# Kernel tuning notes

Hardware: AMD Instinct MI355X
Metric: run time of the kernel (lower is better)

Reference implementation:

```python
import jax, jax.numpy as jnp
import numpy as np

D, B, L, E, H, F = 6, 4, 2048, 1024, 16, 4096
DH = E // H
DECAY = 16.0
CSCALE = 1.0
EPS = 1e-5


def _ln(x, w, b):
    m = jnp.mean(x, axis=-1, keepdims=True)
    v = jnp.mean(jnp.square(x - m), axis=-1, keepdims=True)
    return (x - m) * jax.lax.rsqrt(v + EPS) * w + b


def setup_inputs() -> dict:
    key = jax.random.key(0)
    ks = jax.random.split(key, 10)
    s = 0.02
    f32 = jnp.float32
    return {
        "x": jax.random.normal(ks[0], (B, L, E), f32),
        "Wq": jax.random.normal(ks[1], (D, E, E), f32) * s,
        "Wk": jax.random.normal(ks[2], (D, E, E), f32) * s,
        "bq": jnp.zeros((D, E), f32),
        "bk": jnp.zeros((D, E), f32),
        "ln1_w": jnp.ones((D, E), f32), "ln1_b": jnp.zeros((D, E), f32),
        "ln2_w": jnp.ones((D, E), f32), "ln2_b": jnp.zeros((D, E), f32),
        "ln3_w": jnp.ones((D, E), f32), "ln3_b": jnp.zeros((D, E), f32),
        "W1": jax.random.normal(ks[3], (D, F, E), f32) * s,
        "b1": jnp.zeros((D, F), f32),
        "W2": jax.random.normal(ks[4], (D, E, F), f32) * s,
        "b2": jnp.zeros((D, E), f32),
    }


def reference(x, Wq, Wk, bq, bk, ln1_w, ln1_b, ln2_w, ln2_b, ln3_w, ln3_b, W1, b1, W2, b2):
    seq = x.shape[1]
    pos = jnp.arange(seq)
    # exponential relative-position bias exp(-|i-j|/decay), shared by all layers
    rel = jnp.exp(-jnp.abs(pos[:, None] - pos[None, :]).astype(x.dtype) / DECAY)
    inv_sqrt_d = 1.0 / np.sqrt(DH)

    def layer(h, p):
        (wq, wk, bq_, bk_, l1w, l1b, l2w, l2b, l3w, l3b, w1, b1_, w2, b2_) = p
        bh, sl, _ = h.shape
        q = (h @ wq.T + bq_).reshape(bh, sl, H, DH)
        k = (h @ wk.T + bk_).reshape(bh, sl, H, DH)
        scores = jnp.einsum('blhd,bmhd->bhlm', q, k) * inv_sqrt_d
        # torch MHA need_weights=True averages softmax weights over heads
        w_avg = jax.nn.softmax(scores, axis=-1).mean(axis=1)  # [B,L,L]
        new_w = jax.nn.softmax(CSCALE * w_avg + rel[None], axis=-1)
        sa = jnp.einsum('blm,bme->ble', new_w, h)  # value = raw residual stream
        h1 = _ln(h + sa, l1w, l1b)
        h2 = _ln(h1, l2w, l2b)  # Noop cross-attn block (LayerNorm scale-invariant)
        ff = jax.nn.relu(h2 @ w1.T + b1_) @ w2.T + b2_
        return _ln(h2 + ff, l3w, l3b), None

    out, _ = jax.lax.scan(layer, x, (Wq, Wk, bq, bk, ln1_w, ln1_b, ln2_w, ln2_b,
                                     ln3_w, ln3_b, W1, b1, W2, b2))
    return out
```

## Files before the change

### kernel.cpp

```cpp
#include <hip/hip_runtime.h>

#define D_ 6
#define B_ 4
#define L_ 2048
#define E_ 1024
#define H_ 16
#define F_ 4096
#define BL_ (B_ * L_)
#define QKS 2048
#define EPS_ 1e-5f
#define EXPSC 0.18033688011112042f
#define LOG2E 1.4426950408889634f
#define LOG2E_H (LOG2E / 16.0f)

typedef __bf16 bf16x8 __attribute__((ext_vector_type(8)));
typedef __bf16 bf16x4 __attribute__((ext_vector_type(4)));
typedef float f32x4 __attribute__((ext_vector_type(4)));

__device__ __forceinline__ float fexp2(float x) {
  return __builtin_amdgcn_exp2f(x);
}

__device__ __forceinline__ void gload_lds16(const void* g, void* l) {
  __builtin_amdgcn_global_load_lds(
      (const __attribute__((address_space(1))) void*)g,
      (__attribute__((address_space(3))) void*)l, 16, 0, 0);
}

__device__ __forceinline__ void stage_tile64_512(__bf16* ldsb,
                                                 const __bf16* gbase, long ldg,
                                                 int tid) {
  int row = tid >> 3, cu = tid & 7;
  const __bf16* src = gbase + (long)row * ldg + ((cu ^ (row & 7)) << 3);
  gload_lds16(src, ldsb + (long)((tid & ~63) << 3));
}

__device__ __forceinline__ void stage_tile128_512(__bf16* ldsb,
                                                  const __bf16* gbase,
                                                  long ldg, int tid) {
#pragma unroll
  for (int j = 0; j < 2; ++j) {
    int unit = j * 512 + tid;
    int row = unit >> 3, cu = unit & 7;
    const __bf16* src = gbase + (long)row * ldg + ((cu ^ (row & 7)) << 3);
    gload_lds16(src, ldsb + (long)((j * 512 + (tid & ~63)) << 3));
  }
}

#define RD_FRAG(ldsb, r_, kk) \
  (*(const bf16x8*)&(ldsb)[((r_) * 8 + (((kk) * 4 + l4) ^ ((r_) & 7))) * 8])

#define LDA_SUB(P, MH)                                                        \
  _Pragma("unroll") for (int mi = 0; mi < 4; ++mi)                            \
  _Pragma("unroll") for (int kk = 0; kk < 2; ++kk) {                          \
    int r_ = wr + (MH) * 64 + mi * 16 + l15;                                  \
    int cu_ = kk * 4 + l4;                                                    \
    aF[mi][kk] = *(const bf16x8*)&lds[P][0][(r_ * 8 + (cu_ ^ (r_ & 7))) * 8]; \
  }

#define LDB_SUB(P, BF, NH)                                                    \
  _Pragma("unroll") for (int ni = 0; ni < 2; ++ni)                            \
  _Pragma("unroll") for (int kk = 0; kk < 2; ++kk) {                          \
    int r_ = wc + (NH) * 32 + ni * 16 + l15;                                  \
    int cu_ = kk * 4 + l4;                                                    \
    BF[ni][kk] = *(const bf16x8*)&lds[P][1][(r_ * 8 + (cu_ ^ (r_ & 7))) * 8]; \
  }

#define MFMA_Q(AF, BF, MH, NH)                                                \
  _Pragma("unroll") for (int mi = 0; mi < 4; ++mi)                            \
  _Pragma("unroll") for (int ni = 0; ni < 2; ++ni)                            \
  _Pragma("unroll") for (int kk = 0; kk < 2; ++kk)                            \
    acc[(MH) * 4 + mi][(NH) * 2 + ni] =                                       \
        __builtin_amdgcn_mfma_f32_16x16x32_bf16(                              \
            AF[mi][kk], BF[ni][kk], acc[(MH) * 4 + mi][(NH) * 2 + ni], 0, 0, 0);

#define PHASE_PRE()                                                           \
  __builtin_amdgcn_s_barrier();                                               \
  asm volatile("s_waitcnt lgkmcnt(0)" ::: "memory");                          \
  __builtin_amdgcn_sched_barrier(0);                                          \
  __builtin_amdgcn_s_setprio(1)

#define PHASE_POST()                                                          \
  __builtin_amdgcn_s_setprio(0);                                              \
  __builtin_amdgcn_sched_barrier(0);                                          \
  __builtin_amdgcn_s_barrier()

#define STAGE_A(BUFI, HF, K0)                                                 \
  do {                                                                        \
    gload_lds16(sA[HF][0] + (K0),                                             \
                &lds[BUFI][0][((HF) * 1024 + wave * 64) * 8]);                \
    gload_lds16(sA[HF][1] + (K0),                                             \
                &lds[BUFI][0][((HF) * 1024 + 512 + wave * 64) * 8]);          \
  } while (0)

#define STAGE_B(BUFI, HF, K0)                                                 \
  do {                                                                        \
    gload_lds16(sB[HF][0] + (K0),                                             \
                &lds[BUFI][1][((HF) * 1024 + wave * 64) * 8]);                \
    gload_lds16(sB[HF][1] + (K0),                                             \
                &lds[BUFI][1][((HF) * 1024 + 512 + wave * 64) * 8]);          \
  } while (0)

template <int EPI>
__global__ __launch_bounds__(512, 2) void gemm8p(
    const __bf16* __restrict__ A, const __bf16* __restrict__ Bm,
    __bf16* __restrict__ Cb, const float* __restrict__ bias, int M, int N,
    int K, int lda, int ldb, int zk, long strA, long strB, long strC,
    long strCk) {
  __shared__ __bf16 lds[2][2][256 * 64];
  const int tid = threadIdx.x;
  const int wave = tid >> 6, lane = tid & 63;
  const int l15 = lane & 15, l4 = lane >> 4;
  const int z = blockIdx.y;
  const int kc = (zk == 2) ? (z & 1) : 0;
  const int bat = (zk == 2) ? (z >> 1) : z;
  const __bf16* Ab = A + (long)bat * strA + (long)kc * K;
  const __bf16* Bb = Bm + (long)bat * strB + (long)kc * K;
  const long coff = (long)bat * strC + (long)kc * strCk;

  const int nbx = N >> 8;
  const int nwg = (M >> 8) * nbx;
  const int orig = blockIdx.x;
  const int qq = nwg >> 3, rr = nwg & 7;
  const int xcd = orig & 7, lid = orig >> 3;
  const int wg = (xcd < rr ? xcd * (qq + 1) : rr * (qq + 1) + (xcd - rr) * qq) + lid;
  const int row0 = (wg / nbx) * 256, col0 = (wg % nbx) * 256;
  const int wr = (wave >> 2) * 128;
  const int wc = (wave & 3) * 64;

  const int rsel = tid >> 3;
  const int swz = ((lane & 7) ^ (rsel & 7)) << 3;
  const __bf16* sA[2][2];
  const __bf16* sB[2][2];
#pragma unroll
  for (int hf = 0; hf < 2; ++hf)
#pragma unroll
    for (int j = 0; j < 2; ++j) {
      sA[hf][j] = Ab + (long)(row0 + hf * 128 + j * 64 + rsel) * lda + swz;
      sB[hf][j] = Bb + (long)(col0 + hf * 128 + j * 64 + rsel) * ldb + swz;
    }

  const int NT = K >> 6;
  STAGE_A(0, 0, 0);
  STAGE_A(0, 1, 0);
  STAGE_B(0, 0, 0);
  STAGE_B(0, 1, 0);
  STAGE_A(1, 0, 64);
  STAGE_B(1, 0, 64);
  STAGE_A(1, 1, 64);
  asm volatile("s_waitcnt vmcnt(6)" ::: "memory");
  __builtin_amdgcn_s_barrier();

  f32x4 acc[8][4];
#pragma unroll
  for (int i = 0; i < 8; ++i)
#pragma unroll
    for (int j = 0; j < 4; ++j) acc[i][j] = (f32x4){0.f, 0.f, 0.f, 0.f};
  bf16x8 aF[4][2], b0F[2][2], b1F[2][2];

  for (int t = 0; t < NT; ++t) {
    const int p = t & 1;
    const int kA = (t + 1 < NT ? t + 1 : NT - 1) << 6;
    const int kB = (t + 2 < NT ? t + 2 : NT - 1) << 6;
    LDA_SUB(p, 0);
    LDB_SUB(p, b0F, 0);
    STAGE_B(p ^ 1, 1, kA);
    PHASE_PRE();
    MFMA_Q(aF, b0F, 0, 0);
    PHASE_POST();
    LDB_SUB(p, b1F, 1);
    PHASE_PRE();
    MFMA_Q(aF, b1F, 0, 1);
    PHASE_POST();
    LDA_SUB(p, 1);
    STAGE_B(p, 0, kB);
    PHASE_PRE();
    MFMA_Q(aF, b0F, 1, 0);
    PHASE_POST();
    STAGE_A(p, 0, kB);
    STAGE_A(p, 1, kB);
    __builtin_amdgcn_s_barrier();
    __builtin_amdgcn_sched_barrier(0);
    __builtin_amdgcn_s_setprio(1);
    MFMA_Q(aF, b1F, 1, 1);
    __builtin_amdgcn_s_setprio(0);
    __builtin_amdgcn_sched_barrier(0);
    asm volatile("s_waitcnt vmcnt(6)" ::: "memory");
    __builtin_amdgcn_s_barrier();
  }
  asm volatile("s_waitcnt vmcnt(0)" ::: "memory");

#pragma unroll
  for (int i = 0; i < 8; ++i) {
    int row = row0 + wr + (i >> 2) * 64 + (i & 3) * 16 + l4 * 4;
#pragma unroll
    for (int j = 0; j < 4; ++j) {
      int col = col0 + wc + (j >> 1) * 32 + (j & 1) * 16 + l15;
      float bval = 0.f;
      if constexpr (EPI == 1 || EPI == 2) bval = bias[col];
#pragma unroll
      for (int r = 0; r < 4; ++r) {
        long crow = row + r;
        float v = acc[i][j][r];
        if constexpr (EPI == 1 || EPI == 2) v += bval;
        if constexpr (EPI == 2) v = fmaxf(v, 0.f);
        Cb[coff + crow * N + col] = (__bf16)v;
      }
    }
  }
}

__global__ __launch_bounds__(512, 4) void attn_stats_kernel(
    const __bf16* __restrict__ qk, float* __restrict__ sinv) {
  __shared__ __bf16 sK[2][64 * 64];
  const int tid = threadIdx.x, wave = tid >> 6, lane = tid & 63;
  const int l15 = lane & 15, l4 = lane >> 4;
  const int l0 = blockIdx.x * 128, h = blockIdx.y, b = blockIdx.z;
  const __bf16* Kb = qk + ((long)b * L_) * QKS + 1024 + h * 64;

  const __bf16* qp =
      qk + ((long)(b * L_ + l0 + wave * 16 + l15)) * QKS + h * 64 + l4 * 8;
  const bf16x8 aF0 = *(const bf16x8*)qp;
  const bf16x8 aF1 = *(const bf16x8*)(qp + 32);

  stage_tile64_512(sK[0], Kb, QKS, tid);
  asm volatile("s_waitcnt vmcnt(0)" ::: "memory");
  __builtin_amdgcn_s_barrier();

  float msum[4] = {0.f, 0.f, 0.f, 0.f};
  int p = 0;
  for (int m0 = 0; m0 < 32; ++m0) {
    const int mn = (m0 + 1 < 32) ? m0 + 1 : 31;
    stage_tile64_512(sK[p ^ 1], Kb + (long)mn * 64 * QKS, QKS, tid);
    asm volatile("s_waitcnt vmcnt(1)" ::: "memory");
    __builtin_amdgcn_s_barrier();
#pragma unroll
    for (int ni = 0; ni < 4; ++ni) {
      const int rB = ni * 16 + l15;
      bf16x8 b0 = RD_FRAG(sK[p], rB, 0);
      bf16x8 b1 = RD_FRAG(sK[p], rB, 1);
      f32x4 s = (f32x4){0.f, 0.f, 0.f, 0.f};
      s = __builtin_amdgcn_mfma_f32_16x16x32_bf16(aF0, b0, s, 0, 0, 0);
      s = __builtin_amdgcn_mfma_f32_16x16x32_bf16(aF1, b1, s, 0, 0, 0);
#pragma unroll
      for (int r = 0; r < 4; ++r) msum[r] += fexp2(s[r]);
    }
    asm volatile("" ::: "memory");
    __builtin_amdgcn_s_barrier();
    p ^= 1;
  }
#pragma unroll
  for (int r = 0; r < 4; ++r) {
    float s = msum[r];
    for (int d = 1; d < 16; d <<= 1) s += __shfl_xor(s, d, 64);
    msum[r] = s;
  }
  if (l15 == 0) {
    long idx = ((long)(b * H_ + h)) * L_ + l0 + wave * 16 + l4 * 4;
    f32x4 o = {1.0f / msum[0], 1.0f / msum[1], 1.0f / msum[2], 1.0f / msum[3]};
    *(f32x4*)&sinv[idx] = o;
  }
}

__global__ __launch_bounds__(512, 2) void attn_probs_kernel(
    const __bf16* __restrict__ qk, const float* __restrict__ sinv,
    const float* __restrict__ relTab, __bf16* __restrict__ P,
    float* __restrict__ rowsumT) {
  __shared__ __bf16 sKl[2][128 * 64];
  const int tid = threadIdx.x, wave = tid >> 6, lane = tid & 63;
  const int l15 = lane & 15, l4 = lane >> 4;
  const int m0 = blockIdx.x * 128, l0 = blockIdx.y * 128, b = blockIdx.z;
  const int wr2 = wave & 3, wc2 = wave >> 2;
  const __bf16* Kb = qk + ((long)(b * L_ + m0)) * QKS + 1024;

  const int rowbase = l0 + wr2 * 32 + l4 * 4;
  const __bf16* qp0 =
      qk + ((long)(b * L_ + l0 + wr2 * 32 + l15)) * QKS + l4 * 8;
  const __bf16* qp1 = qp0 + 16 * QKS;

  stage_tile128_512(sKl[0], Kb, QKS, tid);

  float wacc[4][8];
#pragma unroll
  for (int i = 0; i < 4; ++i)
#pragma unroll
    for (int j = 0; j < 8; ++j) wacc[i][j] = 0.f;

  int p = 0;
  for (int h = 0; h < H_; ++h) {
    bf16x8 aF[2][2];
    aF[0][0] = *(const bf16x8*)(qp0 + h * 64);
    aF[0][1] = *(const bf16x8*)(qp0 + h * 64 + 32);
    aF[1][0] = *(const bf16x8*)(qp1 + h * 64);
    aF[1][1] = *(const bf16x8*)(qp1 + h * 64 + 32);
    const float* svh = &sinv[((long)(b * H_ + h)) * L_];
    f32x4 iv0 = *(const f32x4*)&svh[rowbase];
    f32x4 iv1 = *(const f32x4*)&svh[rowbase + 16];
    const int hn = (h + 1 < H_) ? h + 1 : H_ - 1;
    stage_tile128_512(sKl[p ^ 1], Kb + hn * 64, QKS, tid);
    asm volatile("s_waitcnt vmcnt(2)" ::: "memory");
    __builtin_amdgcn_s_barrier();
#pragma unroll
    for (int ni = 0; ni < 4; ++ni) {
      const int rB = wc2 * 64 + ni * 16 + l15;
      bf16x8 b0 = RD_FRAG(sKl[p], rB, 0);
      bf16x8 b1 = RD_FRAG(sKl[p], rB, 1);
#pragma unroll
      for (int fi = 0; fi < 2; ++fi) {
        f32x4 s = (f32x4){0.f, 0.f, 0.f, 0.f};
        s = __builtin_amdgcn_mfma_f32_16x16x32_bf16(aF[fi][0], b0, s, 0, 0, 0);
        s = __builtin_amdgcn_mfma_f32_16x16x32_bf16(aF[fi][1], b1, s, 0, 0, 0);
#pragma unroll
        for (int r = 0; r < 4; ++r)
          wacc[ni][fi * 4 + r] += fexp2(s[r]) * (fi ? iv1[r] : iv0[r]);
      }
    }
    asm volatile("" ::: "memory");
    __builtin_amdgcn_s_barrier();
    p ^= 1;
  }
  float rowpart[2][4] = {{0.f, 0.f, 0.f, 0.f}, {0.f, 0.f, 0.f, 0.f}};
#pragma unroll
  for (int ni = 0; ni < 4; ++ni) {
#pragma unroll
    for (int fi = 0; fi < 2; ++fi) {
#pragma unroll
      for (int r = 0; r < 4; ++r) {
        int row = rowbase + fi * 16 + r;
        int col = m0 + wc2 * 64 + ni * 16 + l15;
        float relL = relTab[row - col + 2048];
        float pv = fexp2(fmaf(wacc[ni][fi * 4 + r], LOG2E_H, relL));
        P[((long)b * L_ + row) * L_ + col] = (__bf16)pv;
        rowpart[fi][r] += pv;
      }
    }
  }
#pragma unroll
  for (int fi = 0; fi < 2; ++fi) {
#pragma unroll
    for (int r = 0; r < 4; ++r) {
      float s = rowpart[fi][r];
      s += __shfl_xor(s, 1, 16);
      s += __shfl_xor(s, 2, 16);
      s += __shfl_xor(s, 4, 16);
      s += __shfl_xor(s, 8, 16);
      if (l15 == 0) {
        int row = rowbase + fi * 16 + r;
        rowsumT[((long)b * L_ + row) * 32 + (m0 >> 6) + wc2] = s;
      }
    }
  }
}

__device__ __forceinline__ void wave_reduce2(float& a, float& b) {
#pragma unroll
  for (int d = 1; d < 64; d <<= 1) {
    a += __shfl_xor(a, d, 64);
    b += __shfl_xor(b, d, 64);
  }
}

__global__ __launch_bounds__(256, 4) void ln12_kernel(
    const float* __restrict__ hin, const __bf16* __restrict__ p0,
    const __bf16* __restrict__ p1, const float* __restrict__ rowsumT,
    const float* __restrict__ w1, const float* __restrict__ b1,
    const float* __restrict__ w2, const float* __restrict__ b2,
    float* __restrict__ h2f, __bf16* __restrict__ h2b) {
  __shared__ float sh[9];
  const int tid = threadIdx.x;
  const long row = blockIdx.x;
  const long base = row * E_ + tid * 4;
  if (tid < 32) {
    float s = rowsumT[row * 32 + tid];
#pragma unroll
    for (int d = 1; d < 32; d <<= 1) s += __shfl_xor(s, d, 32);
    if (tid == 0) sh[8] = s;
  }
  f32x4 hv = *(const f32x4*)&hin[base];
  bf16x4 p0v = *(const bf16x4*)&p0[base];
  bf16x4 p1v = *(const bf16x4*)&p1[base];
  __syncthreads();
  const float rinv = 1.0f / sh[8];
  float y[4];
  float s1 = 0.f, s2 = 0.f;
#pragma unroll
  for (int j = 0; j < 4; ++j) {
    y[j] = hv[j] + rinv * ((float)p0v[j] + (float)p1v[j]);
    s1 += y[j];
    s2 += y[j] * y[j];
  }
  wave_reduce2(s1, s2);
  if ((tid & 63) == 0) { sh[(tid >> 6) * 2] = s1; sh[(tid >> 6) * 2 + 1] = s2; }
  __syncthreads();
  s1 = sh[0] + sh[2] + sh[4] + sh[6];
  s2 = sh[1] + sh[3] + sh[5] + sh[7];
  float mean = s1 * (1.f / E_);
  float var = s2 * (1.f / E_) - mean * mean;
  float rs = rsqrtf(var + EPS_);
  f32x4 wv = *(const f32x4*)&w1[tid * 4];
  f32x4 bv = *(const f32x4*)&b1[tid * 4];
  float h1[4];
  s1 = 0.f; s2 = 0.f;
#pragma unroll
  for (int j = 0; j < 4; ++j) {
    h1[j] = (y[j] - mean) * rs * wv[j] + bv[j];
    s1 += h1[j];
    s2 += h1[j] * h1[j];
  }
  __syncthreads();
  wave_reduce2(s1, s2);
  if ((tid & 63) == 0) { sh[(tid >> 6) * 2] = s1; sh[(tid >> 6) * 2 + 1] = s2; }
  __syncthreads();
  s1 = sh[0] + sh[2] + sh[4] + sh[6];
  s2 = sh[1] + sh[3] + sh[5] + sh[7];
  mean = s1 * (1.f / E_);
  var = s2 * (1.f / E_) - mean * mean;
  rs = rsqrtf(var + EPS_);
  wv = *(const f32x4*)&w2[tid * 4];
  bv = *(const f32x4*)&b2[tid * 4];
  f32x4 o;
  bf16x4 ob;
#pragma unroll
  for (int j = 0; j < 4; ++j) {
    float v = (h1[j] - mean) * rs * wv[j] + bv[j];
    o[j] = v;
    ob[j] = (__bf16)v;
  }
  *(f32x4*)&h2f[base] = o;
  *(bf16x4*)&h2b[base] = ob;
}

__global__ __launch_bounds__(256, 4) void ln3_kernel(
    const float* __restrict__ h2f, const __bf16* __restrict__ p0,
    const __bf16* __restrict__ p1, const float* __restrict__ bias2,
    const float* __restrict__ w3, const float* __restrict__ b3,
    float* __restrict__ outf, __bf16* __restrict__ outb) {
  __shared__ float sh[8];
  const int tid = threadIdx.x;
  const long row = blockIdx.x;
  const long base = row * E_ + tid * 4;
  f32x4 hv = *(const f32x4*)&h2f[base];
  bf16x4 p0v = *(const bf16x4*)&p0[base];
  bf16x4 p1v = *(const bf16x4*)&p1[base];
  f32x4 b2v = *(const f32x4*)&bias2[tid * 4];
  float y[4];
  float s1 = 0.f, s2 = 0.f;
#pragma unroll
  for (int j = 0; j < 4; ++j) {
    y[j] = hv[j] + (float)p0v[j] + (float)p1v[j] + b2v[j];
    s1 += y[j];
    s2 += y[j] * y[j];
  }
  wave_reduce2(s1, s2);
  if ((tid & 63) == 0) { sh[(tid >> 6) * 2] = s1; sh[(tid >> 6) * 2 + 1] = s2; }
  __syncthreads();
  s1 = sh[0] + sh[2] + sh[4] + sh[6];
  s2 = sh[1] + sh[3] + sh[5] + sh[7];
  float mean = s1 * (1.f / E_);
  float var = s2 * (1.f / E_) - mean * mean;
  float rs = rsqrtf(var + EPS_);
  f32x4 wv = *(const f32x4*)&w3[tid * 4];
  f32x4 bv = *(const f32x4*)&b3[tid * 4];
  f32x4 o;
  bf16x4 ob;
#pragma unroll
  for (int j = 0; j < 4; ++j) {
    float v = (y[j] - mean) * rs * wv[j] + bv[j];
    o[j] = v;
    ob[j] = (__bf16)v;
  }
  *(f32x4*)&outf[base] = o;
  *(bf16x4*)&outb[base] = ob;
}

__global__ __launch_bounds__(256, 4) void transpose_kernel(
    const __bf16* __restrict__ X, __bf16* __restrict__ XT) {
  __shared__ __bf16 t[64 * 66];
  const int l0 = blockIdx.x * 64, e0 = blockIdx.y * 64, b = blockIdx.z;
  const int tid = threadIdx.x;
#pragma unroll
  for (int r = 0; r < 2; ++r) {
    int c = tid + 256 * r;
    int rw = c >> 3, c8 = (c & 7) * 8;
    *(bf16x8*)&t[rw * 66 + c8] =
        *(const bf16x8*)&X[((long)(b * L_) + l0 + rw) * E_ + e0 + c8];
  }
  __syncthreads();
#pragma unroll
  for (int r = 0; r < 2; ++r) {
    int c = tid + 256 * r;
    int er = c >> 3, l8 = (c & 7) * 8;
    bf16x8 v;
#pragma unroll
    for (int j = 0; j < 8; ++j) v[j] = t[(l8 + j) * 66 + er];
    *(bf16x8*)&XT[((long)(b * E_) + e0 + er) * L_ + l0 + l8] = v;
  }
}

__global__ __launch_bounds__(256, 4) void f32_to_bf16_kernel(
    const float* __restrict__ x, __bf16* __restrict__ y) {
  long i = ((long)blockIdx.x * 256 + threadIdx.x) * 4;
  f32x4 v = *(const f32x4*)&x[i];
  bf16x4 o;
#pragma unroll
  for (int j = 0; j < 4; ++j) o[j] = (__bf16)v[j];
  *(bf16x4*)&y[i] = o;
}

__global__ __launch_bounds__(256, 4) void build_wqk_kernel(
    const float* __restrict__ Wq, const float* __restrict__ Wk,
    __bf16* __restrict__ out) {
  long i = ((long)blockIdx.x * 256 + threadIdx.x) * 4;
  long d = i >> 21;
  long rem = i & ((1L << 21) - 1);
  long row = rem >> 10, col = rem & 1023;
  const bool isQ = (row < 1024);
  const float* src = isQ ? &Wq[(d << 20) + (row << 10) + col]
                         : &Wk[(d << 20) + ((row - 1024) << 10) + col];
  const float sc = isQ ? EXPSC : 1.0f;
  f32x4 v = *(const f32x4*)src;
  bf16x4 o;
#pragma unroll
  for (int j = 0; j < 4; ++j) o[j] = (__bf16)(v[j] * sc);
  *(bf16x4*)&out[i] = o;
}

__global__ __launch_bounds__(256, 4) void build_bqk_kernel(
    const float* __restrict__ bq, const float* __restrict__ bk,
    float* __restrict__ out) {
  int i = blockIdx.x * 256 + threadIdx.x;
  int d = i >> 11, c = i & 2047;
  out[i] = (c < 1024) ? bq[d * 1024 + c] * EXPSC : bk[d * 1024 + c - 1024];
}

__global__ __launch_bounds__(256, 4) void build_rel_kernel(
    float* __restrict__ relTab) {
  int i = blockIdx.x * 256 + threadIdx.x;
  relTab[i] = __expf(-fabsf((float)(i - 2048)) * (1.0f / 16.0f)) * LOG2E;
}

extern "C" void kernel_launch(void* const* d_in, const int* in_sizes, int n_in,
                              void* d_out, int out_size, void* d_ws,
                              size_t ws_size, hipStream_t stream) {
  const float* x = (const float*)d_in[0];
  const float* Wq = (const float*)d_in[1];
  const float* Wk = (const float*)d_in[2];
  const float* bq = (const float*)d_in[3];
  const float* bk = (const float*)d_in[4];
  const float* l1w = (const float*)d_in[5];
  const float* l1b = (const float*)d_in[6];
  const float* l2w = (const float*)d_in[7];
  const float* l2b = (const float*)d_in[8];
  const float* l3w = (const float*)d_in[9];
  const float* l3b = (const float*)d_in[10];
  const float* W1 = (const float*)d_in[11];
  const float* b1 = (const float*)d_in[12];
  const float* W2 = (const float*)d_in[13];
  const float* b2 = (const float*)d_in[14];

  char* p = (char*)d_ws;
  auto take = [&](size_t bytes) -> char* {
    char* r = p;
    p += (bytes + 255) & ~(size_t)255;
    return r;
  };
  __bf16* wqk_bf = (__bf16*)take((size_t)D_ * 2048 * 1024 * 2);
  __bf16* w1_bf = (__bf16*)take((size_t)D_ * F_ * E_ * 2);
  __bf16* w2_bf = (__bf16*)take((size_t)D_ * E_ * F_ * 2);
  __bf16* h_bf = (__bf16*)take((size_t)BL_ * E_ * 2);
  __bf16* hT = (__bf16*)take((size_t)BL_ * E_ * 2);
  __bf16* qk_bf = (__bf16*)take((size_t)BL_ * QKS * 2);
  __bf16* Pbuf = (__bf16*)take((size_t)B_ * L_ * L_ * 2);
  __bf16* ffmid = qk_bf;
  float* bqk = (float*)take((size_t)D_ * 2048 * 4);
  float* relTab = (float*)take((size_t)4096 * 4);
  float* sinv = (float*)take((size_t)B_ * H_ * L_ * 4);
  float* rowsumT = (float*)take((size_t)BL_ * 32 * 4);
  __bf16* partB = (__bf16*)take((size_t)2 * BL_ * E_ * 2);
  __bf16* part0 = partB;
  __bf16* part1 = partB + (size_t)BL_ * E_;
  float* hbuf = (float*)take((size_t)BL_ * E_ * 4);

  build_wqk_kernel<<<D_ * 2048 * 1024 / 1024, 256, 0, stream>>>(Wq, Wk, wqk_bf);
  build_bqk_kernel<<<D_ * 2048 / 256, 256, 0, stream>>>(bq, bk, bqk);
  build_rel_kernel<<<16, 256, 0, stream>>>(relTab);
  f32_to_bf16_kernel<<<D_ * F_ * E_ / 1024, 256, 0, stream>>>(W1, w1_bf);
  f32_to_bf16_kernel<<<D_ * E_ * F_ / 1024, 256, 0, stream>>>(W2, w2_bf);
  f32_to_bf16_kernel<<<BL_ * E_ / 1024, 256, 0, stream>>>(x, h_bf);
  transpose_kernel<<<dim3(L_ / 64, E_ / 64, B_), 256, 0, stream>>>(h_bf, hT);

  const float* h_in = x;
  for (int d = 0; d < D_; ++d) {
    gemm8p<1><<<dim3(256, 1), 512, 0, stream>>>(
        h_bf, wqk_bf + (size_t)d * 2048 * 1024, qk_bf, bqk + d * 2048, BL_,
        2048, E_, E_, E_, 1, 0, 0, 0, 0);
    attn_stats_kernel<<<dim3(L_ / 128, H_, B_), 512, 0, stream>>>(qk_bf, sinv);
    attn_probs_kernel<<<dim3(L_ / 128, L_ / 128, B_), 512, 0, stream>>>(
        qk_bf, sinv, relTab, Pbuf, rowsumT);
    gemm8p<0><<<dim3(32, 8), 512, 0, stream>>>(
        Pbuf, hT, partB, nullptr, L_, E_, L_ / 2, L_, L_, 2, (long)L_ * L_,
        (long)E_ * L_, (long)L_ * E_, (long)BL_ * E_);
    ln12_kernel<<<BL_, 256, 0, stream>>>(h_in, part0, part1, rowsumT,
                                         l1w + d * E_, l1b + d * E_,
                                         l2w + d * E_, l2b + d * E_, hbuf,
                                         h_bf);
    gemm8p<2><<<dim3(512, 1), 512, 0, stream>>>(
        h_bf, w1_bf + (size_t)d * F_ * E_, ffmid, b1 + d * F_, BL_, F_, E_,
        E_, E_, 1, 0, 0, 0, 0);
    gemm8p<0><<<dim3(128, 2), 512, 0, stream>>>(
        ffmid, w2_bf + (size_t)d * E_ * F_, partB, nullptr, BL_, E_, F_ / 2,
        F_, F_, 2, 0, 0, 0, (long)BL_ * E_);
    float* outp = (d == D_ - 1) ? (float*)d_out : hbuf;
    ln3_kernel<<<BL_, 256, 0, stream>>>(hbuf, part0, part1, b2 + d * E_,
                                        l3w + d * E_, l3b + d * E_, outp,
                                        h_bf);
    if (d < D_ - 1) {
      transpose_kernel<<<dim3(L_ / 64, E_ / 64, B_), 256, 0, stream>>>(h_bf, hT);
      h_in = hbuf;
    }
  }
}
```

Baseline: 2.379 ms.

## Stage Q tiles through LDS in attn_probs and drop fp32 h2 residual buffer

The attention-probability kernel now double-buffers Q head slices into shared memory alongside K, replacing strided per-lane global loads of Q fragments with async LDS staging. Separately, ln12 no longer writes an fp32 copy of h2, and ln3 reads the bf16 h2 for the residual instead. This cuts global traffic in both places. The cost is doubled LDS use in attn_probs, which may reduce occupancy, and lower precision of the residual in the final layer norm.

```diff
diff --git a/kernel.cpp b/kernel.cpp
--- a/kernel.cpp
+++ b/kernel.cpp
@@ -266,40 +266,41 @@
     const __bf16* __restrict__ qk, const float* __restrict__ sinv,
     const float* __restrict__ relTab, __bf16* __restrict__ P,
     float* __restrict__ rowsumT) {
+  __shared__ __bf16 sQ[2][128 * 64];
   __shared__ __bf16 sKl[2][128 * 64];
   const int tid = threadIdx.x, wave = tid >> 6, lane = tid & 63;
   const int l15 = lane & 15, l4 = lane >> 4;
   const int m0 = blockIdx.x * 128, l0 = blockIdx.y * 128, b = blockIdx.z;
   const int wr2 = wave & 3, wc2 = wave >> 2;
+  const __bf16* Qb = qk + ((long)(b * L_ + l0)) * QKS;
   const __bf16* Kb = qk + ((long)(b * L_ + m0)) * QKS + 1024;
 
+  stage_tile128_512(sQ[0], Qb, QKS, tid);
+  stage_tile128_512(sKl[0], Kb, QKS, tid);
+
+  float wacc[4][8];
+#pragma unroll
+  for (int i = 0; i < 4; ++i)
+#pragma unroll
+    for (int j = 0; j < 8; ++j) wacc[i][j] = 0.f;
+
+  const int rA0 = wr2 * 32 + l15;
   const int rowbase = l0 + wr2 * 32 + l4 * 4;
-  const __bf16* qp0 =
-      qk + ((long)(b * L_ + l0 + wr2 * 32 + l15)) * QKS + l4 * 8;
-  const __bf16* qp1 = qp0 + 16 * QKS;
-
-  stage_tile128_512(sKl[0], Kb, QKS, tid);
-
-  float wacc[4][8];
-#pragma unroll
-  for (int i = 0; i < 4; ++i)
-#pragma unroll
-    for (int j = 0; j < 8; ++j) wacc[i][j] = 0.f;
-
   int p = 0;
   for (int h = 0; h < H_; ++h) {
-    bf16x8 aF[2][2];
-    aF[0][0] = *(const bf16x8*)(qp0 + h * 64);
-    aF[0][1] = *(const bf16x8*)(qp0 + h * 64 + 32);
-    aF[1][0] = *(const bf16x8*)(qp1 + h * 64);
-    aF[1][1] = *(const bf16x8*)(qp1 + h * 64 + 32);
+    const int hn = (h + 1 < H_) ? h + 1 : H_ - 1;
+    stage_tile128_512(sQ[p ^ 1], Qb + hn * 64, QKS, tid);
+    stage_tile128_512(sKl[p ^ 1], Kb + hn * 64, QKS, tid);
     const float* svh = &sinv[((long)(b * H_ + h)) * L_];
     f32x4 iv0 = *(const f32x4*)&svh[rowbase];
     f32x4 iv1 = *(const f32x4*)&svh[rowbase + 16];
-    const int hn = (h + 1 < H_) ? h + 1 : H_ - 1;
-    stage_tile128_512(sKl[p ^ 1], Kb + hn * 64, QKS, tid);
-    asm volatile("s_waitcnt vmcnt(2)" ::: "memory");
+    asm volatile("s_waitcnt vmcnt(4)" ::: "memory");
     __builtin_amdgcn_s_barrier();
+    bf16x8 aF[2][2];
+    aF[0][0] = RD_FRAG(sQ[p], rA0, 0);
+    aF[0][1] = RD_FRAG(sQ[p], rA0, 1);
+    aF[1][0] = RD_FRAG(sQ[p], rA0 + 16, 0);
+    aF[1][1] = RD_FRAG(sQ[p], rA0 + 16, 1);
 #pragma unroll
     for (int ni = 0; ni < 4; ++ni) {
       const int rB = wc2 * 64 + ni * 16 + l15;
@@ -365,7 +366,7 @@
     const __bf16* __restrict__ p1, const float* __restrict__ rowsumT,
     const float* __restrict__ w1, const float* __restrict__ b1,
     const float* __restrict__ w2, const float* __restrict__ b2,
-    float* __restrict__ h2f, __bf16* __restrict__ h2b) {
+    __bf16* __restrict__ h2b) {
   __shared__ float sh[9];
   const int tid = threadIdx.x;
   const long row = blockIdx.x;
@@ -418,20 +419,15 @@
   rs = rsqrtf(var + EPS_);
   wv = *(const f32x4*)&w2[tid * 4];
   bv = *(const f32x4*)&b2[tid * 4];
-  f32x4 o;
   bf16x4 ob;
 #pragma unroll
-  for (int j = 0; j < 4; ++j) {
-    float v = (h1[j] - mean) * rs * wv[j] + bv[j];
-    o[j] = v;
-    ob[j] = (__bf16)v;
-  }
-  *(f32x4*)&h2f[base] = o;
+  for (int j = 0; j < 4; ++j)
+    ob[j] = (__bf16)((h1[j] - mean) * rs * wv[j] + bv[j]);
   *(bf16x4*)&h2b[base] = ob;
 }
 
 __global__ __launch_bounds__(256, 4) void ln3_kernel(
-    const float* __restrict__ h2f, const __bf16* __restrict__ p0,
+    const __bf16* __restrict__ h2b_in, const __bf16* __restrict__ p0,
     const __bf16* __restrict__ p1, const float* __restrict__ bias2,
     const float* __restrict__ w3, const float* __restrict__ b3,
     float* __restrict__ outf, __bf16* __restrict__ outb) {
@@ -439,7 +435,7 @@
   const int tid = threadIdx.x;
   const long row = blockIdx.x;
   const long base = row * E_ + tid * 4;
-  f32x4 hv = *(const f32x4*)&h2f[base];
+  bf16x4 hv = *(const bf16x4*)&h2b_in[base];
   bf16x4 p0v = *(const bf16x4*)&p0[base];
   bf16x4 p1v = *(const bf16x4*)&p1[base];
   f32x4 b2v = *(const f32x4*)&bias2[tid * 4];
@@ -447,7 +443,7 @@
   float s1 = 0.f, s2 = 0.f;
 #pragma unroll
   for (int j = 0; j < 4; ++j) {
-    y[j] = hv[j] + (float)p0v[j] + (float)p1v[j] + b2v[j];
+    y[j] = (float)hv[j] + (float)p0v[j] + (float)p1v[j] + b2v[j];
     s1 += y[j];
     s2 += y[j] * y[j];
   }
@@ -602,8 +598,7 @@
         (long)E_ * L_, (long)L_ * E_, (long)BL_ * E_);
     ln12_kernel<<<BL_, 256, 0, stream>>>(h_in, part0, part1, rowsumT,
                                          l1w + d * E_, l1b + d * E_,
-                                         l2w + d * E_, l2b + d * E_, hbuf,
-                                         h_bf);
+                                         l2w + d * E_, l2b + d * E_, h_bf);
     gemm8p<2><<<dim3(512, 1), 512, 0, stream>>>(
         h_bf, w1_bf + (size_t)d * F_ * E_, ffmid, b1 + d * F_, BL_, F_, E_,
         E_, E_, 1, 0, 0, 0, 0);
@@ -611,7 +606,7 @@
         ffmid, w2_bf + (size_t)d * E_ * F_, partB, nullptr, BL_, E_, F_ / 2,
         F_, F_, 2, 0, 0, 0, (long)BL_ * E_);
     float* outp = (d == D_ - 1) ? (float*)d_out : hbuf;
-    ln3_kernel<<<BL_, 256, 0, stream>>>(hbuf, part0, part1, b2 + d * E_,
+    ln3_kernel<<<BL_, 256, 0, stream>>>(h_bf, part0, part1, b2 + d * E_,
                                         l3w + d * E_, l3b + d * E_, outp,
                                         h_bf);
     if (d < D_ - 1) {
```

After: 2.205 ms. -7.3%, faster.
